# Kernel optimization log

Measured on AMD Instinct MI355X. Metric: run time of the kernel, lower is better.

## Reference

```python
import jax, jax.numpy as jnp
import numpy as np

NEG = -1000000000.0  # mask value used by the original module

def setup_inputs() -> dict:
    key = jax.random.key(0)
    kq, kk, kv, kl = jax.random.split(key, 4)
    B, Lq, Lk, D, Dv = 16, 2048, 2048, 64, 64
    q = jax.random.normal(kq, (B, Lq, D), dtype=jnp.float32)
    k = jax.random.normal(kk, (B, Lk, D), dtype=jnp.float32)
    v = jax.random.normal(kv, (B, Lk, Dv), dtype=jnp.float32)
    valid_len = jax.random.randint(kl, (B, Lq), 0, Lk, dtype=jnp.int32)
    return {"q": q, "k": k, "v": v, "valid_len": valid_len}

def reference(q, k, v, valid_len):
    # scores: [B, Lq, Lk]  (NOTE: original module does NOT scale by sqrt(d))
    scores = jnp.einsum('bqd,bkd->bqk', q, k)
    Lk = k.shape[1]
    # per-(batch,query) valid length masking over the key dimension
    mask = jnp.arange(Lk, dtype=valid_len.dtype)[None, None, :] < valid_len[:, :, None]
    scores = jnp.where(mask, scores, NEG)
    attn = jax.nn.softmax(scores, axis=-1)
    # dropout p=0.0 -> identity
    return jnp.einsum('bqk,bkv->bqv', attn, v)
```

## Files before the change

kernel.cpp:

```cpp
#include <hip/hip_runtime.h>

typedef _Float16 f16;
typedef unsigned long long ull;
typedef __attribute__((ext_vector_type(8))) _Float16 f16x8;
typedef __attribute__((ext_vector_type(4))) _Float16 f16x4;
typedef __attribute__((ext_vector_type(4))) float f32x4;

#define NB 16
#define LSEQ 2048
#define DIM 64
#define KVB 64
#define QT 128
#define NQT (LSEQ / QT)
#define NT (LSEQ / KVB)
#define LOG2E 1.44269504088896340736f

union PU4 { ull u; f16x4 v; };
union PU8 { ull u[2]; f16x8 v; };

__device__ inline f16x4 pkcvt(const f32x4 x) {
    auto a = __builtin_amdgcn_cvt_pkrtz(x[0], x[1]);
    auto b = __builtin_amdgcn_cvt_pkrtz(x[2], x[3]);
    f16x4 t; t[0]=(f16)a[0]; t[1]=(f16)a[1]; t[2]=(f16)b[0]; t[3]=(f16)b[1];
    return t;
}

__device__ inline void gload16(const void* g, void* l) {
    __builtin_amdgcn_global_load_lds(
        (const __attribute__((address_space(1))) unsigned int*)g,
        (__attribute__((address_space(3))) unsigned int*)l, 16, 0, 0);
}

__global__ __launch_bounds__(256) void prep(
    const float* __restrict__ kg, const float* __restrict__ vg,
    const int* __restrict__ vlg,
    f16* __restrict__ k16, f16* __restrict__ v16, int* __restrict__ perm)
{
    const int tid = threadIdx.x;
    if (blockIdx.x < NB * NT) {
        const int b = blockIdx.x & 15, t = blockIdx.x >> 4;
        const int bt = b * NT + t;
        const float* kb_ = kg + ((size_t)b * LSEQ + t * KVB) * DIM;
        const float* vb_ = vg + ((size_t)b * LSEQ + t * KVB) * DIM;
        f16* kd = k16 + (size_t)bt * (KVB * DIM);
        f16* vd = v16 + (size_t)bt * (KVB * DIM);
#pragma unroll
        for (int it = 0; it < 4; ++it) {
            int cc = tid + it * 256;
            int row = cc >> 4, c4 = (cc & 15) * 4;
            f32x4 x = *(const f32x4*)(kb_ + row * DIM + c4);
            *(f16x4*)(kd + row * 64 + (c4 ^ ((row & 7) * 8))) = pkcvt(x);
        }
        int kb4 = tid & 15, dvb = tid >> 4;
        f32x4 rr[4];
#pragma unroll
        for (int i = 0; i < 4; ++i)
            rr[i] = *(const f32x4*)(vb_ + (size_t)(kb4 * 4 + i) * DIM + dvb * 4);
#pragma unroll
        for (int j = 0; j < 4; ++j) {
            int dv = dvb * 4 + j;
            f32x4 col = {rr[0][j], rr[1][j], rr[2][j], rr[3][j]};
            *(f16x4*)(vd + dv * 64 + ((kb4 * 4) ^ ((dv & 7) * 8))) = pkcvt(col);
        }
    } else {
        const int b = blockIdx.x - NB * NT;
        __shared__ int hist[NT + 1];
        __shared__ int base[NT + 1];
        if (tid <= NT) hist[tid] = 0;
        __syncthreads();
        for (int q = tid; q < LSEQ; q += 256) {
            int vl = vlg[b * LSEQ + q];
            int t = (vl == 0) ? NT : ((vl + KVB - 1) >> 6);
            atomicAdd(&hist[t], 1);
        }
        __syncthreads();
        if (tid == 0) {
            int acc = 0;
            for (int t = NT; t >= 0; --t) { base[t] = acc; acc += hist[t]; }
        }
        __syncthreads();
        for (int q = tid; q < LSEQ; q += 256) {
            int vl = vlg[b * LSEQ + q];
            int t = (vl == 0) ? NT : ((vl + KVB - 1) >> 6);
            int pos = atomicAdd(&base[t], 1);
            perm[b * LSEQ + pos] = q;
        }
    }
}

__global__ __launch_bounds__(256, 4) void attn_fwd(
    const float* __restrict__ qg, const int* __restrict__ vlg,
    const f16* __restrict__ k16, const f16* __restrict__ v16,
    float* __restrict__ outg, const int* __restrict__ perm,
    f16* __restrict__ opart, float* __restrict__ mlg, int S)
{
    __shared__ alignas(16) f16 kbuf[2][KVB * 64];
    __shared__ alignas(16) f16 vbuf[2][DIM * 64];
    __shared__ int wmax[4];

    const int tid  = threadIdx.x;
    const int wid  = tid >> 6;
    const int lane = tid & 63;
    const int r    = lane & 15;
    const int hi   = lane >> 4;

    const int bid = blockIdx.x;
    const int nbs = NB * S;
    const int qt  = bid / nbs;
    const int rem = bid - qt * nbs;
    const int s   = rem >> 4;
    const int b   = rem & 15;
    const int qw  = qt * QT + wid * 16;

    const int qidxA = perm[b * LSEQ + qw + r];
    const int qidxB = perm[b * LSEQ + qw + 64 + r];
    const int vlA   = vlg[b * LSEQ + qidxA];
    const int vlB   = vlg[b * LSEQ + qidxB];

    int tq = max((vlA == 0) ? NT : ((vlA + KVB - 1) >> 6),
                 (vlB == 0) ? NT : ((vlB + KVB - 1) >> 6));
    tq = max(tq, __shfl_xor(tq, 1));
    tq = max(tq, __shfl_xor(tq, 2));
    tq = max(tq, __shfl_xor(tq, 4));
    tq = max(tq, __shfl_xor(tq, 8));
    if (lane == 0) wmax[wid] = tq;
    __syncthreads();
    const int maxt = max(max(wmax[0], wmax[1]), max(wmax[2], wmax[3]));

    auto wave_min = [&](int v) {
        v = min(v, __shfl_xor(v, 1));
        v = min(v, __shfl_xor(v, 2));
        v = min(v, __shfl_xor(v, 4));
        v = min(v, __shfl_xor(v, 8));
        return v;
    };
    const int vminA = wave_min(vlA);
    const int vminB = wave_min(vlB);

    auto load_q = [&](int qidx, f16x8* qf) {
        const float* qrow = qg + ((size_t)(b * LSEQ + qidx)) * DIM;
#pragma unroll
        for (int ks = 0; ks < 2; ++ks) {
            f32x4 x = *(const f32x4*)(qrow + ks * 32 + hi * 8);
            f32x4 y = *(const f32x4*)(qrow + ks * 32 + hi * 8 + 4);
            f32x4 xs = {x[0]*LOG2E, x[1]*LOG2E, x[2]*LOG2E, x[3]*LOG2E};
            f32x4 ys = {y[0]*LOG2E, y[1]*LOG2E, y[2]*LOG2E, y[3]*LOG2E};
            f16x4 lo = pkcvt(xs), hh = pkcvt(ys);
            f16x8 t;
            t[0]=lo[0]; t[1]=lo[1]; t[2]=lo[2]; t[3]=lo[3];
            t[4]=hh[0]; t[5]=hh[1]; t[6]=hh[2]; t[7]=hh[3];
            qf[ks] = t;
        }
    };
    f16x8 qfA[2], qfB[2];
    load_q(qidxA, qfA);
    load_q(qidxB, qfB);

    float mA = -INFINITY, mB = -INFINITY;
    float lA = 0.0f, lB = 0.0f;
    f32x4 oA[4], oB[4];
#pragma unroll
    for (int dt = 0; dt < 4; ++dt) { oA[dt] = f32x4{0,0,0,0}; oB[dt] = f32x4{0,0,0,0}; }

    const f16* kt_base = k16 + (size_t)b * (NT * KVB * DIM);
    const f16* vt_base = v16 + (size_t)b * (NT * KVB * DIM);
    const int swz = (r & 7) * 8;
    const int psrc = r + ((lane & 16) << 1);

    auto stage = [&](int bi, int t) {
        const char* ks = (const char*)(kt_base + (size_t)t * 4096);
        const char* vs = (const char*)(vt_base + (size_t)t * 4096);
        char* kd = (char*)&kbuf[bi][0];
        char* vd = (char*)&vbuf[bi][0];
        gload16(ks + tid * 16,        kd + tid * 16);
        gload16(ks + 4096 + tid * 16, kd + 4096 + tid * 16);
        gload16(vs + tid * 16,        vd + tid * 16);
        gload16(vs + 4096 + tid * 16, vd + 4096 + tid * 16);
    };

    auto do_frag = [&](const f16x8* qf, int vl, int vmin,
                       float& m_run, float& l_run, f32x4* o,
                       int kv0, const f16* kb_, const f16* vb_) {
        f32x4 st[4];
        __builtin_amdgcn_s_setprio(1);
#pragma unroll
        for (int kt = 0; kt < 4; ++kt) {
            f32x4 acc = f32x4{0,0,0,0};
#pragma unroll
            for (int ks = 0; ks < 2; ++ks) {
                f16x8 kf = *(const f16x8*)(&kb_[(kt * 16 + r) * 64 + ((ks * 32 + hi * 8) ^ swz)]);
                acc = __builtin_amdgcn_mfma_f32_16x16x32_f16(kf, qf[ks], acc, 0, 0, 0);
            }
            st[kt] = acc;
        }
        __builtin_amdgcn_s_setprio(0);

        float lanemax = -INFINITY;
        if (kv0 + KVB > vmin) {
#pragma unroll
            for (int kt = 0; kt < 4; ++kt)
#pragma unroll
                for (int g = 0; g < 4; ++g) {
                    int key = kv0 + kt * 16 + hi * 4 + g;
                    float sv = (key < vl) ? st[kt][g] : -1e9f;
                    st[kt][g] = sv;
                    lanemax = fmaxf(lanemax, sv);
                }
        } else {
#pragma unroll
            for (int kt = 0; kt < 4; ++kt)
#pragma unroll
                for (int g = 0; g < 4; ++g)
                    lanemax = fmaxf(lanemax, st[kt][g]);
        }

        if (__any(lanemax > m_run + 8.0f)) {
            float tmax = lanemax;
            tmax = fmaxf(tmax, __shfl_xor(tmax, 16));
            tmax = fmaxf(tmax, __shfl_xor(tmax, 32));
            float m_new = fmaxf(m_run, tmax);
            float scale = exp2f(m_run - m_new);
            l_run *= scale;
            m_run = m_new;
#pragma unroll
            for (int g = 0; g < 4; ++g) {
                float sc = __shfl(scale, hi * 4 + g);
#pragma unroll
                for (int dt = 0; dt < 4; ++dt) o[dt][g] *= sc;
            }
        }

        ull held[4];
#pragma unroll
        for (int kt = 0; kt < 4; ++kt) {
            f16x4 pv;
#pragma unroll
            for (int g = 0; g < 4; ++g) {
                float p = exp2f(st[kt][g] - m_run);
                l_run += p;
                pv[g] = (f16)p;
            }
            PU4 u; u.v = pv; held[kt] = u.u;
        }

        f16x8 pa[2];
#pragma unroll
        for (int ks = 0; ks < 2; ++ks) {
            ull c0 = __shfl(held[2 * ks],     psrc);
            ull c1 = __shfl(held[2 * ks + 1], psrc);
            ull d0 = __shfl(held[2 * ks],     psrc + 16);
            ull d1 = __shfl(held[2 * ks + 1], psrc + 16);
            PU8 u;
            u.u[0] = (hi & 2) ? c1 : c0;
            u.u[1] = (hi & 2) ? d1 : d0;
            pa[ks] = u.v;
        }

        __builtin_amdgcn_s_setprio(1);
#pragma unroll
        for (int ks = 0; ks < 2; ++ks) {
#pragma unroll
            for (int dt = 0; dt < 4; ++dt) {
                f16x8 vf = *(const f16x8*)(&vb_[(dt * 16 + r) * 64 + ((ks * 32 + hi * 8) ^ swz)]);
                o[dt] = __builtin_amdgcn_mfma_f32_16x16x32_f16(pa[ks], vf, o[dt], 0, 0, 0);
            }
        }
        __builtin_amdgcn_s_setprio(0);
    };

    if (s < maxt) stage(0, s);
    int c = 0;
    for (int tt = s; tt < maxt; tt += S) {
        __syncthreads();
        if (tt + S < maxt) stage(c ^ 1, tt + S);
        const int kv0 = tt * KVB;
        do_frag(qfA, vlA, vminA, mA, lA, oA, kv0, &kbuf[c][0], &vbuf[c][0]);
        do_frag(qfB, vlB, vminB, mB, lB, oB, kv0, &kbuf[c][0], &vbuf[c][0]);
        c ^= 1;
    }

    auto epi = [&](float m_run, float l_run, f32x4* o, int qidx) {
        l_run += __shfl_xor(l_run, 16);
        l_run += __shfl_xor(l_run, 32);
        if (S == 1) {
            float inv = 1.0f / l_run;
#pragma unroll
            for (int g = 0; g < 4; ++g) {
                float iv = __shfl(inv, hi * 4 + g);
                int   qo = __shfl(qidx, hi * 4 + g);
                float* ob = outg + ((size_t)(b * LSEQ + qo)) * DIM;
#pragma unroll
                for (int dt = 0; dt < 4; ++dt)
                    ob[dt * 16 + r] = o[dt][g] * iv;
            }
        } else {
            f16* obase = opart + ((size_t)s * NB * LSEQ + (size_t)b * LSEQ) * DIM;
#pragma unroll
            for (int g = 0; g < 4; ++g) {
                int qo = __shfl(qidx, hi * 4 + g);
                f16* ob = obase + (size_t)qo * DIM;
#pragma unroll
                for (int dt = 0; dt < 4; ++dt)
                    ob[dt * 16 + r] = (f16)o[dt][g];
            }
            if (hi == 0) {
                size_t mi = ((size_t)s * NB * LSEQ + (size_t)b * LSEQ + qidx) * 2;
                mlg[mi]     = m_run;
                mlg[mi + 1] = l_run;
            }
        }
    };
    epi(mA, lA, oA, qidxA);
    epi(mB, lB, oB, qidxB);
}

__global__ void merge_k(const f16* __restrict__ opart, const float* __restrict__ mlg,
                        float* __restrict__ outg, int S)
{
    const int gt = blockIdx.x * 256 + threadIdx.x;
    const size_t base = (size_t)gt * 4;
    const size_t qg = base >> 6;
    float M = -INFINITY;
    for (int s = 0; s < S; ++s)
        M = fmaxf(M, mlg[((size_t)s * NB * LSEQ + qg) * 2]);
    float den = 0.f;
    f32x4 acc = {0.f, 0.f, 0.f, 0.f};
    for (int s = 0; s < S; ++s) {
        size_t mi = ((size_t)s * NB * LSEQ + qg) * 2;
        float w = exp2f(mlg[mi] - M);
        den += w * mlg[mi + 1];
        f16x4 ov = *(const f16x4*)(opart + (size_t)s * (NB * LSEQ * DIM) + base);
        acc[0] += w * (float)ov[0]; acc[1] += w * (float)ov[1];
        acc[2] += w * (float)ov[2]; acc[3] += w * (float)ov[3];
    }
    float inv = 1.0f / den;
    f32x4 res = {acc[0]*inv, acc[1]*inv, acc[2]*inv, acc[3]*inv};
    *(f32x4*)(outg + base) = res;
}

extern "C" void kernel_launch(void* const* d_in, const int* in_sizes, int n_in,
                              void* d_out, int out_size, void* d_ws, size_t ws_size,
                              hipStream_t stream) {
    const float* q  = (const float*)d_in[0];
    const float* k  = (const float*)d_in[1];
    const float* v  = (const float*)d_in[2];
    const int*   vl = (const int*)d_in[3];
    float* out = (float*)d_out;

    const size_t perm_b = (size_t)NB * LSEQ * sizeof(int);
    const size_t kv_b   = (size_t)NB * LSEQ * DIM * sizeof(f16);
    auto need = [&](int S) {
        return perm_b + 2 * kv_b
             + (size_t)S * NB * LSEQ * 2 * sizeof(float)
             + (size_t)S * NB * LSEQ * DIM * sizeof(f16);
    };
    int S;
    if      (ws_size >= need(6)) S = 6;
    else if (ws_size >= need(4)) S = 4;
    else if (ws_size >= need(2)) S = 2;
    else                         S = 1;

    int*   perm  = (int*)d_ws;
    f16*   k16   = (f16*)((char*)d_ws + perm_b);
    f16*   v16   = (f16*)((char*)d_ws + perm_b + kv_b);
    float* mlg   = (float*)((char*)d_ws + perm_b + 2 * kv_b);
    f16*   opart = (f16*)((char*)d_ws + perm_b + 2 * kv_b
                          + (size_t)S * NB * LSEQ * 2 * sizeof(float));

    prep<<<NB * NT + NB, 256, 0, stream>>>(k, v, vl, k16, v16, perm);

    attn_fwd<<<dim3(NQT * NB * S), dim3(256), 0, stream>>>(
        q, vl, k16, v16, out, perm, opart, mlg, S);

    if (S > 1) {
        const int mthreads = NB * LSEQ * DIM / 4;
        merge_k<<<dim3(mthreads / 256), dim3(256), 0, stream>>>(opart, mlg, out, S);
    }
}
```

Baseline: 53.15 us.

## Load K/V tiles straight into registers per wave, dropping LDS staging

Each wave now loads its own K and V MFMA fragments directly from global memory into registers with a two-deep register double buffer, replacing block-wide LDS staging and barriers. The prep kernel stops swizzling, since no LDS bank conflicts remain to avoid. Each wave handles 32 contiguous sorted queries and computes its own tile count, so waves with short valid lengths stop early instead of waiting on the block maximum. Occupancy is lowered to 2 blocks per SM to make room for the larger register footprint, and the split factor is capped at 4. K/V global traffic grows about fourfold because tiles are no longer shared across waves, and it must be served from L2.

```diff
diff --git a/kernel.cpp b/kernel.cpp
--- a/kernel.cpp
+++ b/kernel.cpp
@@ -23,12 +23,6 @@
     auto b = __builtin_amdgcn_cvt_pkrtz(x[2], x[3]);
     f16x4 t; t[0]=(f16)a[0]; t[1]=(f16)a[1]; t[2]=(f16)b[0]; t[3]=(f16)b[1];
     return t;
-}
-
-__device__ inline void gload16(const void* g, void* l) {
-    __builtin_amdgcn_global_load_lds(
-        (const __attribute__((address_space(1))) unsigned int*)g,
-        (__attribute__((address_space(3))) unsigned int*)l, 16, 0, 0);
 }
 
 __global__ __launch_bounds__(256) void prep(
@@ -49,7 +43,7 @@
             int cc = tid + it * 256;
             int row = cc >> 4, c4 = (cc & 15) * 4;
             f32x4 x = *(const f32x4*)(kb_ + row * DIM + c4);
-            *(f16x4*)(kd + row * 64 + (c4 ^ ((row & 7) * 8))) = pkcvt(x);
+            *(f16x4*)(kd + row * 64 + c4) = pkcvt(x);
         }
         int kb4 = tid & 15, dvb = tid >> 4;
         f32x4 rr[4];
@@ -60,7 +54,7 @@
         for (int j = 0; j < 4; ++j) {
             int dv = dvb * 4 + j;
             f32x4 col = {rr[0][j], rr[1][j], rr[2][j], rr[3][j]};
-            *(f16x4*)(vd + dv * 64 + ((kb4 * 4) ^ ((dv & 7) * 8))) = pkcvt(col);
+            *(f16x4*)(vd + dv * 64 + kb4 * 4) = pkcvt(col);
         }
     } else {
         const int b = blockIdx.x - NB * NT;
@@ -88,16 +82,12 @@
     }
 }
 
-__global__ __launch_bounds__(256, 4) void attn_fwd(
+__global__ __launch_bounds__(256, 2) void attn_fwd(
     const float* __restrict__ qg, const int* __restrict__ vlg,
     const f16* __restrict__ k16, const f16* __restrict__ v16,
     float* __restrict__ outg, const int* __restrict__ perm,
     f16* __restrict__ opart, float* __restrict__ mlg, int S)
 {
-    __shared__ alignas(16) f16 kbuf[2][KVB * 64];
-    __shared__ alignas(16) f16 vbuf[2][DIM * 64];
-    __shared__ int wmax[4];
-
     const int tid  = threadIdx.x;
     const int wid  = tid >> 6;
     const int lane = tid & 63;
@@ -110,10 +100,10 @@
     const int rem = bid - qt * nbs;
     const int s   = rem >> 4;
     const int b   = rem & 15;
-    const int qw  = qt * QT + wid * 16;
+    const int qw  = qt * QT + wid * 32;
 
     const int qidxA = perm[b * LSEQ + qw + r];
-    const int qidxB = perm[b * LSEQ + qw + 64 + r];
+    const int qidxB = perm[b * LSEQ + qw + 16 + r];
     const int vlA   = vlg[b * LSEQ + qidxA];
     const int vlB   = vlg[b * LSEQ + qidxB];
 
@@ -123,19 +113,17 @@
     tq = max(tq, __shfl_xor(tq, 2));
     tq = max(tq, __shfl_xor(tq, 4));
     tq = max(tq, __shfl_xor(tq, 8));
-    if (lane == 0) wmax[wid] = tq;
-    __syncthreads();
-    const int maxt = max(max(wmax[0], wmax[1]), max(wmax[2], wmax[3]));
-
-    auto wave_min = [&](int v) {
+    const int maxt = tq;
+
+    auto rmin = [&](int v) {
         v = min(v, __shfl_xor(v, 1));
         v = min(v, __shfl_xor(v, 2));
         v = min(v, __shfl_xor(v, 4));
         v = min(v, __shfl_xor(v, 8));
         return v;
     };
-    const int vminA = wave_min(vlA);
-    const int vminB = wave_min(vlB);
+    const int vminA = rmin(vlA);
+    const int vminB = rmin(vlB);
 
     auto load_q = [&](int qidx, f16x8* qf) {
         const float* qrow = qg + ((size_t)(b * LSEQ + qidx)) * DIM;
@@ -162,35 +150,34 @@
 #pragma unroll
     for (int dt = 0; dt < 4; ++dt) { oA[dt] = f32x4{0,0,0,0}; oB[dt] = f32x4{0,0,0,0}; }
 
-    const f16* kt_base = k16 + (size_t)b * (NT * KVB * DIM);
-    const f16* vt_base = v16 + (size_t)b * (NT * KVB * DIM);
-    const int swz = (r & 7) * 8;
+    const int loff = r * 64 + hi * 8;
+    const f16* kt_base = k16 + (size_t)b * (NT * KVB * DIM) + loff;
+    const f16* vt_base = v16 + (size_t)b * (NT * KVB * DIM) + loff;
     const int psrc = r + ((lane & 16) << 1);
 
-    auto stage = [&](int bi, int t) {
-        const char* ks = (const char*)(kt_base + (size_t)t * 4096);
-        const char* vs = (const char*)(vt_base + (size_t)t * 4096);
-        char* kd = (char*)&kbuf[bi][0];
-        char* vd = (char*)&vbuf[bi][0];
-        gload16(ks + tid * 16,        kd + tid * 16);
-        gload16(ks + 4096 + tid * 16, kd + 4096 + tid * 16);
-        gload16(vs + tid * 16,        vd + tid * 16);
-        gload16(vs + 4096 + tid * 16, vd + 4096 + tid * 16);
-    };
-
-    auto do_frag = [&](const f16x8* qf, int vl, int vmin,
-                       float& m_run, float& l_run, f32x4* o,
-                       int kv0, const f16* kb_, const f16* vb_) {
+    auto load_kv = [&](int t, f16x8* kf, f16x8* vf) {
+        const f16* kp = kt_base + (size_t)t * 4096;
+        const f16* vp = vt_base + (size_t)t * 4096;
+#pragma unroll
+        for (int i = 0; i < 4; ++i) {
+#pragma unroll
+            for (int ks = 0; ks < 2; ++ks) {
+                kf[i * 2 + ks] = *(const f16x8*)(kp + i * 1024 + ks * 32);
+                vf[i * 2 + ks] = *(const f16x8*)(vp + i * 1024 + ks * 32);
+            }
+        }
+    };
+
+    auto do_frag = [&](const f16x8* qf, const f16x8* kb, const f16x8* vb,
+                       int vl, int vmin, float& m_run, float& l_run, f32x4* o, int kv0) {
         f32x4 st[4];
         __builtin_amdgcn_s_setprio(1);
 #pragma unroll
         for (int kt = 0; kt < 4; ++kt) {
             f32x4 acc = f32x4{0,0,0,0};
 #pragma unroll
-            for (int ks = 0; ks < 2; ++ks) {
-                f16x8 kf = *(const f16x8*)(&kb_[(kt * 16 + r) * 64 + ((ks * 32 + hi * 8) ^ swz)]);
-                acc = __builtin_amdgcn_mfma_f32_16x16x32_f16(kf, qf[ks], acc, 0, 0, 0);
-            }
+            for (int ks = 0; ks < 2; ++ks)
+                acc = __builtin_amdgcn_mfma_f32_16x16x32_f16(kb[kt * 2 + ks], qf[ks], acc, 0, 0, 0);
             st[kt] = acc;
         }
         __builtin_amdgcn_s_setprio(0);
@@ -258,25 +245,29 @@
 
         __builtin_amdgcn_s_setprio(1);
 #pragma unroll
-        for (int ks = 0; ks < 2; ++ks) {
-#pragma unroll
-            for (int dt = 0; dt < 4; ++dt) {
-                f16x8 vf = *(const f16x8*)(&vb_[(dt * 16 + r) * 64 + ((ks * 32 + hi * 8) ^ swz)]);
-                o[dt] = __builtin_amdgcn_mfma_f32_16x16x32_f16(pa[ks], vf, o[dt], 0, 0, 0);
-            }
-        }
+        for (int ks = 0; ks < 2; ++ks)
+#pragma unroll
+            for (int dt = 0; dt < 4; ++dt)
+                o[dt] = __builtin_amdgcn_mfma_f32_16x16x32_f16(pa[ks], vb[dt * 2 + ks], o[dt], 0, 0, 0);
         __builtin_amdgcn_s_setprio(0);
     };
 
-    if (s < maxt) stage(0, s);
-    int c = 0;
-    for (int tt = s; tt < maxt; tt += S) {
-        __syncthreads();
-        if (tt + S < maxt) stage(c ^ 1, tt + S);
-        const int kv0 = tt * KVB;
-        do_frag(qfA, vlA, vminA, mA, lA, oA, kv0, &kbuf[c][0], &vbuf[c][0]);
-        do_frag(qfB, vlB, vminB, mB, lB, oB, kv0, &kbuf[c][0], &vbuf[c][0]);
-        c ^= 1;
+    f16x8 k0[8], v0[8], k1[8], v1[8];
+    int tt = s;
+    if (tt < maxt) {
+        load_kv(tt, k0, v0);
+        while (true) {
+            if (tt + S < maxt) load_kv(tt + S, k1, v1);
+            do_frag(qfA, k0, v0, vlA, vminA, mA, lA, oA, tt * KVB);
+            do_frag(qfB, k0, v0, vlB, vminB, mB, lB, oB, tt * KVB);
+            tt += S;
+            if (tt >= maxt) break;
+            if (tt + S < maxt) load_kv(tt + S, k0, v0);
+            do_frag(qfA, k1, v1, vlA, vminA, mA, lA, oA, tt * KVB);
+            do_frag(qfB, k1, v1, vlB, vminB, mB, lB, oB, tt * KVB);
+            tt += S;
+            if (tt >= maxt) break;
+        }
     }
 
     auto epi = [&](float m_run, float l_run, f32x4* o, int qidx) {
@@ -355,8 +346,7 @@
              + (size_t)S * NB * LSEQ * DIM * sizeof(f16);
     };
     int S;
-    if      (ws_size >= need(6)) S = 6;
-    else if (ws_size >= need(4)) S = 4;
+    if      (ws_size >= need(4)) S = 4;
     else if (ws_size >= need(2)) S = 2;
     else                         S = 1;
 
```

Result: slower. 77.42 us (+45.7%).
